# Kernel optimization log

Hardware: AMD Instinct MI355X
Metric: run time of the kernel (lower is better)

## Reference

```python
import jax, jax.numpy as jnp
import numpy as np
from jax import lax

DIM = 256
HEAD_DIM = 32
NUM_HEADS = DIM // HEAD_DIM
AGENT = 2
WIN = 7
DN = ('NCHW', 'OIHW', 'NCHW')


def _rpe_index(m, w):
    # faithful to torch buffer construction (meshgrid 'ij')
    coords = np.stack(np.meshgrid(np.arange(m), np.arange(w), np.arange(w), indexing='ij')).reshape(3, -1)
    rel = (coords[:, :, None] - coords[:, None, :]).transpose(1, 2, 0).astype(np.int64)
    rel[..., 0] += m - 1
    rel[..., 1] += w - 1
    rel[..., 2] += w - 1
    rel[..., 0] *= (2 * w - 1) * (2 * w - 1)
    rel[..., 1] *= 2 * w - 1
    return jnp.asarray(rel.sum(-1), dtype=jnp.int32)  # [N, N]


def _feat_extract(x, dw, se1, se2, pw):
    # depthwise 3x3 conv (groups=C, no bias)
    y = lax.conv_general_dilated(x, dw, (1, 1), [(1, 1), (1, 1)], dimension_numbers=DN,
                                 feature_group_count=x.shape[1])
    y = jax.nn.gelu(y, approximate=False)
    # SE block
    s = y.mean(axis=(2, 3))                                   # [B, C]
    s = jax.nn.sigmoid(jax.nn.gelu(s @ se1, approximate=False) @ se2)
    y = y * s[:, :, None, None]
    y = lax.conv_general_dilated(y, pw, (1, 1), [(0, 0), (0, 0)], dimension_numbers=DN)
    x = x + y
    # MaxPool2d(kernel=3, stride=2, padding=1)
    return lax.reduce_window(x, -jnp.inf, lax.max, (1, 1, 3, 3), (1, 1, 2, 2),
                             [(0, 0), (0, 0), (1, 1), (1, 1)])


def setup_inputs() -> dict:
    key = jax.random.key(0)
    ks = jax.random.split(key, 16)
    d, h, hd = DIM, NUM_HEADS, HEAD_DIM
    se_hidden = int(d * 0.25)
    rpe_rows = (2 * AGENT - 1) * (2 * WIN - 1) * (2 * WIN - 1)
    w = lambda k, shp: (jax.random.normal(k, shp, dtype=jnp.float32) * 0.02)
    return {
        'x': jax.random.normal(ks[0], (8, AGENT, 8, 8, WIN, WIN, d), dtype=jnp.float32),
        'qkv_w': w(ks[1], (d, 2 * d)),
        'qkv_b': jnp.zeros((2 * d,), dtype=jnp.float32),
        'to_out_w': w(ks[2], (d, d)),
        'rpe_table': w(ks[3], (rpe_rows, h)),
        'fe1_dw': w(ks[4], (d, 1, 3, 3)),
        'fe1_se1': w(ks[5], (d, se_hidden)),
        'fe1_se2': w(ks[6], (se_hidden, d)),
        'fe1_pw': w(ks[7], (d, d, 1, 1)),
        'fe2_dw': w(ks[8], (d, 1, 3, 3)),
        'fe2_se1': w(ks[9], (d, se_hidden)),
        'fe2_se2': w(ks[10], (se_hidden, d)),
        'fe2_pw': w(ks[11], (d, d, 1, 1)),
    }


def reference(x, qkv_w, qkv_b, to_out_w, rpe_table,
              fe1_dw, fe1_se1, fe1_se2, fe1_pw,
              fe2_dw, fe2_se1, fe2_se2, fe2_pw):
    b, m, gx, gy, w, _, d = x.shape
    h, hd = NUM_HEADS, HEAD_DIM
    scale = hd ** -0.5
    N = m * w * w

    # ---- global query path ----
    # 'b m x y w1 w2 d -> (b m) d (x w1) (y w2)'
    xg = x.transpose(0, 1, 6, 2, 4, 3, 5).reshape(b * m, d, gx * w, gy * w)
    xg = _feat_extract(xg, fe1_dw, fe1_se1, fe1_se2, fe1_pw)
    xg = _feat_extract(xg, fe2_dw, fe2_se1, fe2_se2, fe2_pw)
    C, H, W = xg.shape[1], xg.shape[2], xg.shape[3]
    nx, ny = H // w, W // w
    # '(b m) d (x w1) (y w2) -> b m x y w1 w2 d' then 'b l x y w1 w2 d -> b (x y) (l w1 w2) d'
    xg = xg.reshape(b, m, d, nx, w, ny, w).transpose(0, 3, 5, 1, 4, 6, 2).reshape(b, nx * ny, N, d)
    g_attn = jax.nn.softmax(jnp.einsum('bhid,bhjd->bhij', xg, xg)) * (C ** -0.5)
    xg = jnp.einsum('bhij,bhjd->bhid', g_attn, xg)
    q_global = xg.mean(axis=1)                                 # [b, N, d]
    q_global = q_global.reshape(b, N, h, hd).transpose(0, 2, 1, 3)  # [b, h, N, hd]

    # ---- window attention ----
    # 'b l x y w1 w2 d -> (b x y) (l w1 w2) d'
    xw = x.transpose(0, 2, 3, 1, 4, 5, 6).reshape(b * gx * gy, N, d)
    B_ = xw.shape[0]
    kv = (xw @ qkv_w + qkv_b).reshape(B_, N, 2, h, hd).transpose(2, 0, 3, 1, 4)
    k, v = kv[0], kv[1]                                        # [B_, h, N, hd]
    q = jnp.broadcast_to(q_global[:, None], (b, gx * gy, h, N, hd)).reshape(B_, h, N, hd)

    attn = jnp.einsum('bhid,bhjd->bhij', q * scale, k)         # [B_, h, N, N]
    idx = _rpe_index(m, w)                                     # [N, N] static int32
    bias = rpe_table[idx].transpose(2, 0, 1)                   # [h, N, N]
    attn = jax.nn.softmax(attn + bias[None])
    out = jnp.einsum('bhij,bhjd->bhid', attn, v)               # [B_, h, N, hd]

    # 'b h (l w1 w2) d -> b l w1 w2 (h d)'
    out = out.reshape(B_, h, m, w, w, hd).transpose(0, 2, 3, 4, 1, 5).reshape(B_, m, w, w, d)
    out = out @ to_out_w
    # '(b x y) l w1 w2 d -> b l x y w1 w2 d'
    return out.reshape(b, gx, gy, m, w, w, d).transpose(0, 3, 1, 2, 4, 5, 6)
```

## Files before the change

kernel.cpp:

```cpp
#include <hip/hip_runtime.h>


#define DEV static __device__ __forceinline__
typedef unsigned short u16;
typedef unsigned int u32;
typedef __attribute__((ext_vector_type(8))) short short8;
typedef __attribute__((ext_vector_type(4))) float f32x4;

DEV float b2f(u16 s) { union { u32 i; float f; } u; u.i = ((u32)s) << 16; return u.f; }
DEV u16 f2b(float f) {
    union { float f; u32 i; } u; u.f = f;
    u32 x = u.i;
    return (u16)((x + 0x7fffu + ((x >> 16) & 1u)) >> 16);
}
DEV u16 f2b_hw(float f) {
    __bf16 b = (__bf16)f;
    return __builtin_bit_cast(u16, b);
}
DEV float gelu_f(float x) { return 0.5f * x * (1.0f + erff(x * 0.70710678118654752440f)); }

DEV size_t x_rowbase(int r) {
    int b_ = r / 98, n = r % 98;
    int bb = b_ >> 6, gxi = (b_ >> 3) & 7, gyi = b_ & 7;
    int m = n / 49, rr = n % 49, w1 = rr / 7, w2 = rr % 7;
    return (((((size_t)(bb * 2 + m) * 8 + gxi) * 8 + gyi) * 7 + w1) * 7 + w2) * 256;
}

__global__ __launch_bounds__(256) void k_prep_both(const float* __restrict__ x, u16* __restrict__ xbf,
                                                   float* __restrict__ xg0) {
    int t = threadIdx.x;
    int s = blockIdx.x * 4 + (t >> 6);
    int c4 = (t & 63) << 2;
    int w2 = s % 7, t1 = s / 7;
    int w1 = t1 % 7, t2 = t1 / 7;
    int gy = t2 % 8, t3 = t2 / 8;
    int gx = t3 % 8, nm = t3 / 8;
    int m = nm & 1, bb = nm >> 1;
    int r  = (bb * 64 + gx * 8 + gy) * 98 + m * 49 + w1 * 7 + w2;
    int rg = nm * 3136 + (gx * 7 + w1) * 56 + gy * 7 + w2;
    float4 v = *(const float4*)(x + (size_t)s * 256 + c4);
    ushort4 o; o.x = f2b(v.x); o.y = f2b(v.y); o.z = f2b(v.z); o.w = f2b(v.w);
    *(ushort4*)(xbf + (size_t)r * 256 + c4) = o;
    *(float4*)(xg0 + (size_t)rg * 256 + c4) = v;
}

__global__ __launch_bounds__(256) void k_prep_w(const float* __restrict__ wq, const float* __restrict__ wo,
                                                const float* __restrict__ pw1, const float* __restrict__ pw2,
                                                const float* __restrict__ dw1, const float* __restrict__ dw2,
                                                u16* __restrict__ wqt, u16* __restrict__ wot,
                                                u16* __restrict__ pwb1, u16* __restrict__ pwb2,
                                                float* __restrict__ dwt1, float* __restrict__ dwt2) {
    int bid = blockIdx.x, t = threadIdx.x;
    if (bid < 512) {
        wqt[bid * 256 + t] = f2b(wq[(size_t)t * 512 + bid]);
    } else if (bid < 768) {
        int n = bid - 512;
        wot[n * 256 + t] = f2b(wo[(size_t)t * 256 + n]);
    } else if (bid < 1024) {
        int n = bid - 768;
        pwb1[n * 256 + t] = f2b(pw1[(size_t)n * 256 + t]);
    } else if (bid < 1280) {
        int n = bid - 1024;
        pwb2[n * 256 + t] = f2b(pw2[(size_t)n * 256 + t]);
    } else if (bid < 1289) {
        int k = bid - 1280;
        dwt1[k * 256 + t] = dw1[t * 9 + k];
    } else {
        int k = bid - 1289;
        dwt2[k * 256 + t] = dw2[t * 9 + k];
    }
}

__global__ __launch_bounds__(256) void k_bias(const float* __restrict__ rpe, float* __restrict__ biasf) {
    int u = blockIdx.x * 256 + threadIdx.x;
    int h = u / 10976, rem = u % 10976;
    int i = rem / 112, j = rem % 112;
    float v;
    if (j >= 98) {
        v = -1.0e38f;
    } else {
        int mi = (i >= 49), ri = i - 49 * mi, ai = ri / 7, bi = ri % 7;
        int mj = (j >= 49), rj = j - 49 * mj, aj = rj / 7, bj = rj % 7;
        int idx = ((mi - mj + 1) * 13 + (ai - aj + 6)) * 13 + (bi - bj + 6);
        v = rpe[idx * 8 + h];
    }
    biasf[u] = v;
}

DEV void gemm_tile(const u16* __restrict__ A, const u16* __restrict__ Bt,
                   int r0, int n0, int t, f32x4 acc[4][4],
                   u16 (*A_l)[72], u16 (*B_l)[72]) {
    int w = t >> 6, l = t & 63;
    int quad = l >> 4, lm = l & 15;
    int wm = (w & 1) * 64, wn = (w >> 1) * 64;
    for (int k0 = 0; k0 < 256; k0 += 64) {
        __syncthreads();
        #pragma unroll
        for (int i = 0; i < 4; i++) {
            int u = t + (i << 8);
            int row = u >> 3, k8 = (u & 7) << 3;
            *(uint4*)&A_l[row][k8] = *(const uint4*)(A + (size_t)(r0 + row) * 256 + k0 + k8);
            *(uint4*)&B_l[row][k8] = *(const uint4*)(Bt + (size_t)(n0 + row) * 256 + k0 + k8);
        }
        __syncthreads();
        #pragma unroll
        for (int kk = 0; kk < 64; kk += 32) {
            short8 af[4], bf[4];
            #pragma unroll
            for (int i = 0; i < 4; i++) af[i] = *(const short8*)&A_l[wm + 16 * i + lm][kk + quad * 8];
            #pragma unroll
            for (int j = 0; j < 4; j++) bf[j] = *(const short8*)&B_l[wn + 16 * j + lm][kk + quad * 8];
            #pragma unroll
            for (int i = 0; i < 4; i++)
                #pragma unroll
                for (int j = 0; j < 4; j++)
                    acc[i][j] = __builtin_amdgcn_mfma_f32_16x16x32_bf16(af[i], bf[j], acc[i][j], 0, 0, 0);
        }
    }
}

__global__ __launch_bounds__(256, 2) void k_gemm_qkv(const u16* __restrict__ A, const u16* __restrict__ Bt,
                                                     const float* __restrict__ bias, u16* __restrict__ C) {
    __shared__ u16 A_l[128][72];
    __shared__ u16 B_l[128][72];
    int r0 = blockIdx.x * 128, n0 = blockIdx.y * 128;
    int t = threadIdx.x;
    f32x4 acc[4][4] = {};
    gemm_tile(A, Bt, r0, n0, t, acc, A_l, B_l);
    int w = t >> 6, l = t & 63;
    int quad = l >> 4, lm = l & 15;
    int wm = (w & 1) * 64, wn = (w >> 1) * 64;
    float bj[4];
    #pragma unroll
    for (int j = 0; j < 4; j++) bj[j] = bias[n0 + wn + 16 * j + lm];
    #pragma unroll
    for (int i = 0; i < 4; i++) {
        int rbase = r0 + wm + 16 * i + quad * 4;
        #pragma unroll
        for (int reg = 0; reg < 4; reg++) {
            int row = rbase + reg;
            #pragma unroll
            for (int j = 0; j < 4; j++) {
                int c0 = n0 + wn + 16 * j;
                int slab = c0 >> 5;
                int dd = c0 & 31;
                C[((size_t)slab * 50176 + row) * 32 + dd + lm] = f2b(acc[i][j][reg] + bj[j]);
            }
        }
    }
}

__global__ __launch_bounds__(256, 2) void k_gemm_toout(const u16* __restrict__ A, const u16* __restrict__ Bt,
                                                       float* __restrict__ outp) {
    __shared__ u16 A_l[128][72];
    __shared__ u16 B_l[128][72];
    int r0 = blockIdx.x * 128, n0 = blockIdx.y * 128;
    int t = threadIdx.x;
    f32x4 acc[4][4] = {};
    gemm_tile(A, Bt, r0, n0, t, acc, A_l, B_l);
    int w = t >> 6, l = t & 63;
    int quad = l >> 4, lm = l & 15;
    int wm = (w & 1) * 64, wn = (w >> 1) * 64;
    #pragma unroll
    for (int i = 0; i < 4; i++) {
        int rbase = r0 + wm + 16 * i + quad * 4;
        #pragma unroll
        for (int reg = 0; reg < 4; reg++) {
            size_t ob = x_rowbase(rbase + reg);
            #pragma unroll
            for (int j = 0; j < 4; j++)
                outp[ob + n0 + wn + 16 * j + lm] = acc[i][j][reg];
        }
    }
}

__global__ __launch_bounds__(256) void k_scale_w(const u16* __restrict__ pwb, const float* __restrict__ ubuf,
                                                 u16* __restrict__ pwsc) {
    int b = blockIdx.x;
    int n = b >> 8, co = b & 255;
    int ci = threadIdx.x;
    pwsc[((size_t)b) * 256 + ci] = f2b(b2f(pwb[co * 256 + ci]) * ubuf[n * 256 + ci]);
}

template<int HW>
__global__ __launch_bounds__(256, 2) void k_pwconv_mfma_t(const u16* __restrict__ yT, const u16* __restrict__ pwsc,
                                                          float* __restrict__ base) {
    __shared__ u16 A_l[128][72];
    __shared__ u16 B_l[128][72];
    const int PX = (HW + 127) >> 7;
    int cpx = gridDim.x >> 3;
    int bid = (blockIdx.x & 7) * cpx + (blockIdx.x >> 3);
    int c0 = (bid & 1) * 128;
    int rem = bid >> 1;
    int p0 = (rem % PX) * 128;
    int n  = rem / PX;
    int t = threadIdx.x;
    const u16* A = yT + (size_t)n * HW * 256;
    const u16* Bt = pwsc + (size_t)n * 65536;
    f32x4 acc[4][4] = {};
    gemm_tile(A, Bt, p0, c0, t, acc, A_l, B_l);
    int w = t >> 6, l = t & 63;
    int quad = l >> 4, lm = l & 15;
    int wm = (w & 1) * 64, wn = (w >> 1) * 64;
    #pragma unroll
    for (int i = 0; i < 4; i++) {
        int pb = p0 + wm + 16 * i + quad * 4;
        #pragma unroll
        for (int reg = 0; reg < 4; reg++) {
            int p = pb + reg;
            if (p < HW) {
                size_t rowb = ((size_t)n * HW + p) * 256;
                #pragma unroll
                for (int j = 0; j < 4; j++)
                    base[rowb + c0 + wn + 16 * j + lm] += acc[i][j][reg];
            }
        }
    }
}

__global__ __launch_bounds__(256, 4) void k_attn_mfma(const u16* __restrict__ kv, const u16* __restrict__ qg,
                                                      const float* __restrict__ biasf, u16* __restrict__ ao) {
    __shared__ u16 K_l[112][40];
    __shared__ u16 Vt_l[32][136];
    __shared__ u16 P_l[4][16][136];
    int b_ = blockIdx.x, h = blockIdx.y;
    int bb = b_ >> 6;
    int t = threadIdx.x;

    const u16* kq = kv + ((size_t)h * 50176 + (size_t)b_ * 98) * 32;
    const u16* kvv = kv + ((size_t)(8 + h) * 50176 + (size_t)b_ * 98) * 32;
    const u16* qgn = qg + ((size_t)(bb * 8 + h) * 98) * 32;

    for (int u = t; u < 392; u += 256) {
        int row = u >> 2, q8 = (u & 3) << 3;
        *(short8*)&K_l[row][q8] = *(const short8*)(kq + u * 8);
    }
    for (int u = t; u < 224; u += 256) {
        int row = 98 + (u >> 4), c2 = (u & 15) << 1;
        *(u32*)&K_l[row][c2] = 0;
    }
    for (int u = t; u < 392; u += 256) {
        int j = u >> 2, c = u & 3;
        short8 v = *(const short8*)(kvv + u * 8);
        #pragma unroll
        for (int e = 0; e < 8; e++) Vt_l[c * 8 + e][j] = (u16)v[e];
    }
    for (int u = t; u < 1216; u += 256) {
        int d = u / 38, c = 98 + u % 38;
        Vt_l[d][c] = 0;
    }
    for (int u = t; u < 1536; u += 256) {
        int wv = u / 384, rem = u % 384;
        P_l[wv][rem / 24][112 + rem % 24] = 0;
    }
    __syncthreads();

    int w = t >> 6, l = t & 63;
    int quad = l >> 4, lm = l & 15;
    const float scale = 0.17677669529663688f;

    #pragma unroll
    for (int half = 0; half < 2; half++) {
        int mt = w + 4 * half;
        if (mt >= 7) break;
        int m0 = mt * 16;
        int qrow = m0 + lm; qrow = (qrow < 98) ? qrow : 97;
        const float* bp = biasf + (size_t)(h * 98 + qrow) * 112 + quad * 4;
        f32x4 b4[7];
        #pragma unroll
        for (int t6 = 0; t6 < 7; t6++) b4[t6] = *(const f32x4*)(bp + t6 * 16);
        short8 aq = *(const short8*)(qgn + qrow * 32 + quad * 8);
        f32x4 acc[7] = {};
        #pragma unroll
        for (int t6 = 0; t6 < 7; t6++) {
            short8 bk = *(const short8*)&K_l[t6 * 16 + lm][quad * 8];
            acc[t6] = __builtin_amdgcn_mfma_f32_16x16x32_bf16(bk, aq, acc[t6], 0, 0, 0);
        }
        float mx = -3.0e38f;
        #pragma unroll
        for (int t6 = 0; t6 < 7; t6++) {
            #pragma unroll
            for (int reg = 0; reg < 4; reg++) {
                float s = acc[t6][reg] * scale + b4[t6][reg];
                acc[t6][reg] = s;
                mx = fmaxf(mx, s);
            }
        }
        mx = fmaxf(mx, __shfl_xor(mx, 16));
        mx = fmaxf(mx, __shfl_xor(mx, 32));
        float sum = 0.f;
        #pragma unroll
        for (int t6 = 0; t6 < 7; t6++) {
            #pragma unroll
            for (int reg = 0; reg < 4; reg++) {
                float e = __expf(acc[t6][reg] - mx);
                acc[t6][reg] = e; sum += e;
            }
        }
        sum += __shfl_xor(sum, 16);
        sum += __shfl_xor(sum, 32);
        float inv = 1.0f / sum;
        #pragma unroll
        for (int t6 = 0; t6 < 7; t6++) {
            ushort4 s4;
            s4.x = f2b_hw(acc[t6][0] * inv);
            s4.y = f2b_hw(acc[t6][1] * inv);
            s4.z = f2b_hw(acc[t6][2] * inv);
            s4.w = f2b_hw(acc[t6][3] * inv);
            *(ushort4*)&P_l[w][lm][t6 * 16 + quad * 4] = s4;
        }
        __builtin_amdgcn_s_waitcnt(0);
        short8 pa[4];
        #pragma unroll
        for (int kc = 0; kc < 4; kc++)
            pa[kc] = *(const short8*)&P_l[w][lm][kc * 32 + quad * 8];
        #pragma unroll
        for (int nt = 0; nt < 2; nt++) {
            f32x4 oacc = {};
            #pragma unroll
            for (int kc = 0; kc < 4; kc++) {
                short8 bv = *(const short8*)&Vt_l[nt * 16 + lm][kc * 32 + quad * 8];
                oacc = __builtin_amdgcn_mfma_f32_16x16x32_bf16(pa[kc], bv, oacc, 0, 0, 0);
            }
            #pragma unroll
            for (int reg = 0; reg < 4; reg++) {
                int orow = m0 + quad * 4 + reg;
                if (orow < 98)
                    ao[((size_t)(b_ * 98 + orow)) * 256 + h * 32 + nt * 16 + lm] = f2b_hw(oacc[reg]);
            }
        }
    }
}

template<int HW, int WW>
__global__ __launch_bounds__(256) void k_dwconv_t(const float* __restrict__ in, const float* __restrict__ dwT,
                                                  u16* __restrict__ out) {
    const int HP = HW / 2;
    const int WP = WW / 2;
    int cpx = gridDim.x >> 3;
    int bid = (blockIdx.x & 7) * cpx + (blockIdx.x >> 3);
    int idx = bid * 256 + threadIdx.x;
    int c4 = (idx & 63) << 2;
    int pp = (idx >> 6) % HP;
    int n  = (idx >> 6) / HP;
    int i  = pp / WP, jp = (pp % WP) * 2;
    const float* base = in + (size_t)n * HW * 256 + c4;
    f32x4 w0[3], w1[3], w2[3];
    #pragma unroll
    for (int dy = 0; dy < 3; dy++) {
        w0[dy] = *(const f32x4*)(dwT + (dy * 3 + 0) * 256 + c4);
        w1[dy] = *(const f32x4*)(dwT + (dy * 3 + 1) * 256 + c4);
        w2[dy] = *(const f32x4*)(dwT + (dy * 3 + 2) * 256 + c4);
    }
    f32x4 acc0 = {}, acc1 = {};
    #pragma unroll
    for (int dy = 0; dy < 3; dy++) {
        int y = i + dy - 1;
        if (y < 0 || y >= WW) continue;
        const float* rowb = base + (size_t)(y * WW) * 256;
        f32x4 v1 = *(const f32x4*)(rowb + (size_t)jp * 256);
        f32x4 v2 = *(const f32x4*)(rowb + (size_t)(jp + 1) * 256);
        f32x4 v0 = (jp > 0) ? *(const f32x4*)(rowb + (size_t)(jp - 1) * 256) : (f32x4){};
        f32x4 v3 = (jp + 2 < WW) ? *(const f32x4*)(rowb + (size_t)(jp + 2) * 256) : (f32x4){};
        acc0 += v0 * w0[dy] + v1 * w1[dy] + v2 * w2[dy];
        acc1 += v1 * w0[dy] + v2 * w1[dy] + v3 * w2[dy];
    }
    ushort4 o0, o1;
    o0.x = f2b(gelu_f(acc0[0])); o0.y = f2b(gelu_f(acc0[1]));
    o0.z = f2b(gelu_f(acc0[2])); o0.w = f2b(gelu_f(acc0[3]));
    o1.x = f2b(gelu_f(acc1[0])); o1.y = f2b(gelu_f(acc1[1]));
    o1.z = f2b(gelu_f(acc1[2])); o1.w = f2b(gelu_f(acc1[3]));
    size_t ob = ((size_t)n * HW + (size_t)i * WW + jp) * 256 + c4;
    *(ushort4*)(out + ob) = o0;
    *(ushort4*)(out + ob + 256) = o1;
}

template<int HW>
__global__ __launch_bounds__(256) void k_chanmean_t(const u16* __restrict__ y, float* __restrict__ sbuf) {
    int n = blockIdx.x, sl = blockIdx.y;
    int c = threadIdx.x;
    const int PP = HW / 16;
    const u16* base = y + ((size_t)n * HW + sl * PP) * 256 + c;
    float s = 0.f;
    for (int p = 0; p < PP; p++) s += b2f(base[(size_t)p * 256]);
    atomicAdd(&sbuf[n * 256 + c], s);
}

__global__ __launch_bounds__(256) void k_se1(const float* __restrict__ sbuf, const float* __restrict__ se1,
                                             float* __restrict__ tbuf, float invHW) {
    int o = blockIdx.x * 256 + threadIdx.x;
    int n = o >> 6, j = o & 63;
    const float* srow = sbuf + n * 256;
    float acc = 0.f;
    for (int c = 0; c < 256; c++) acc += srow[c] * se1[c * 64 + j];
    tbuf[o] = gelu_f(acc * invHW);
}
__global__ __launch_bounds__(256) void k_se2(const float* __restrict__ tbuf, const float* __restrict__ se2,
                                             float* __restrict__ ubuf) {
    int o = blockIdx.x * 256 + threadIdx.x;
    int n = o >> 8, co = o & 255;
    const float* trow = tbuf + n * 64;
    float acc = 0.f;
    for (int j = 0; j < 64; j++) acc += trow[j] * se2[j * 256 + co];
    ubuf[o] = 1.0f / (1.0f + __expf(-acc));
}

template<int HI>
__global__ __launch_bounds__(256) void k_maxpool_t(const float* __restrict__ in, float* __restrict__ out) {
    const int HO = HI / 2;
    int cpx = gridDim.x >> 3;
    int bid = (blockIdx.x & 7) * cpx + (blockIdx.x >> 3);
    int idx = bid * 256 + threadIdx.x;
    int c4 = (idx & 63) << 2;
    int pp = (idx >> 6) % (HO * HO);
    int n = (idx >> 6) / (HO * HO);
    int j = pp % HO, i = pp / HO;
    const float* base = in + (size_t)n * HI * HI * 256 + c4;
    float mx = -3.0e38f, my = -3.0e38f, mz = -3.0e38f, mw = -3.0e38f;
    #pragma unroll
    for (int dr = 0; dr < 3; dr++) {
        int r = 2 * i - 1 + dr;
        if (r < 0 || r >= HI) continue;
        #pragma unroll
        for (int dc = 0; dc < 3; dc++) {
            int cc = 2 * j - 1 + dc;
            if (cc < 0 || cc >= HI) continue;
            float4 v = *(const float4*)(base + (size_t)(r * HI + cc) * 256);
            mx = fmaxf(mx, v.x); my = fmaxf(my, v.y);
            mz = fmaxf(mz, v.z); mw = fmaxf(mw, v.w);
        }
    }
    float4 o; o.x = mx; o.y = my; o.z = mz; o.w = mw;
    *(float4*)(out + (size_t)idx * 4) = o;
}

__global__ __launch_bounds__(256) void k_rearr_xg_t(const float* __restrict__ p2, float* __restrict__ xg) {
    int t = threadIdx.x;
    int r = blockIdx.x * 4 + (t >> 6);
    int c4 = (t & 63) << 2;
    int gihi = r / 98, n = r % 98;
    int b = gihi >> 2, gi = gihi & 3;
    int m = n / 49, rr = n % 49, w1 = rr / 7, w2 = rr % 7;
    int X = (gi >> 1) * 7 + w1, Y = (gi & 1) * 7 + w2;
    size_t src = ((size_t)((b * 2 + m) * 196 + X * 14 + Y)) * 256;
    *(float4*)(xg + (size_t)r * 256 + c4) = *(const float4*)(p2 + src + c4);
}

__global__ __launch_bounds__(256, 2) void k_gattn(const float* __restrict__ xg, float* __restrict__ qpart) {
    int rt = blockIdx.x, gi = blockIdx.y, b = blockIdx.z;
    __shared__ float A_l[98][68];
    __shared__ float S_l[14][100];
    int t = threadIdx.x;
    const float* Ab = xg + (size_t)(b * 4 + gi) * 98 * 256;
    int ti = t >> 5, tj = t & 31;
    int i1c = (ti + 8 < 14) ? ti + 8 : 13;
    int jc[4];
    #pragma unroll
    for (int jj = 0; jj < 4; jj++) { int j = tj + 32 * jj; jc[jj] = (j < 98) ? j : 97; }
    float accS[2][4] = {};
    for (int ch = 0; ch < 4; ch++) {
        __syncthreads();
        for (int u = t; u < 1568; u += 256) {
            int row = u >> 4, c4 = (u & 15) << 2;
            *(float4*)&A_l[row][c4] = *(const float4*)(Ab + row * 256 + ch * 64 + c4);
        }
        __syncthreads();
        for (int c4 = 0; c4 < 64; c4 += 4) {
            float4 ak[4];
            #pragma unroll
            for (int jj = 0; jj < 4; jj++) ak[jj] = *(const float4*)&A_l[jc[jj]][c4];
            float4 aq0 = *(const float4*)&A_l[rt * 14 + ti][c4];
            float4 aq1 = *(const float4*)&A_l[rt * 14 + i1c][c4];
            #pragma unroll
            for (int jj = 0; jj < 4; jj++) {
                accS[0][jj] += aq0.x * ak[jj].x + aq0.y * ak[jj].y + aq0.z * ak[jj].z + aq0.w * ak[jj].w;
                accS[1][jj] += aq1.x * ak[jj].x + aq1.y * ak[jj].y + aq1.z * ak[jj].z + aq1.w * ak[jj].w;
            }
        }
    }
    #pragma unroll
    for (int ii = 0; ii < 2; ii++) {
        int il = ti + 8 * ii;
        if (il < 14) {
            #pragma unroll
            for (int jj = 0; jj < 4; jj++) {
                int j = tj + 32 * jj;
                if (j < 98) S_l[il][j] = accS[ii][jj];
            }
        }
    }
    __syncthreads();
    {
        int g = t >> 4, l = t & 15;
        if (g < 14) {
            float mx = -3.0e38f;
            for (int jj = 0; jj < 7; jj++) { int j = l + 16 * jj; if (j < 98) mx = fmaxf(mx, S_l[g][j]); }
            #pragma unroll
            for (int off = 8; off > 0; off >>= 1) mx = fmaxf(mx, __shfl_xor(mx, off, 16));
            float sum = 0.f;
            for (int jj = 0; jj < 7; jj++) {
                int j = l + 16 * jj;
                if (j < 98) { float e = __expf(S_l[g][j] - mx); S_l[g][j] = e; sum += e; }
            }
            #pragma unroll
            for (int off = 8; off > 0; off >>= 1) sum += __shfl_xor(sum, off, 16);
            float inv = 0.0625f / sum;
            for (int jj = 0; jj < 7; jj++) { int j = l + 16 * jj; if (j < 98) S_l[g][j] *= inv; }
        }
    }
    __syncthreads();
    int ti2 = t >> 4, tc2 = t & 15;
    int rowv = (ti2 < 14);
    int ti2c = rowv ? ti2 : 13;
    size_t qrow = ((size_t)(b * 4 + gi) * 98 + rt * 14 + ti2c) * 256;
    for (int ch = 0; ch < 4; ch++) {
        __syncthreads();
        for (int u = t; u < 1568; u += 256) {
            int row = u >> 4, c4 = (u & 15) << 2;
            *(float4*)&A_l[row][c4] = *(const float4*)(Ab + row * 256 + ch * 64 + c4);
        }
        __syncthreads();
        float4 acc = make_float4(0.f, 0.f, 0.f, 0.f);
        for (int j0 = 0; j0 < 96; j0 += 4) {
            float s4[4];
            *(float4*)s4 = *(const float4*)&S_l[ti2c][j0];
            #pragma unroll
            for (int jj = 0; jj < 4; jj++) {
                float4 a = *(const float4*)&A_l[j0 + jj][tc2 * 4];
                acc.x += s4[jj] * a.x; acc.y += s4[jj] * a.y; acc.z += s4[jj] * a.z; acc.w += s4[jj] * a.w;
            }
        }
        #pragma unroll
        for (int j = 96; j < 98; j++) {
            float sv = S_l[ti2c][j];
            float4 a = *(const float4*)&A_l[j][tc2 * 4];
            acc.x += sv * a.x; acc.y += sv * a.y; acc.z += sv * a.z; acc.w += sv * a.w;
        }
        if (rowv) *(float4*)(qpart + qrow + ch * 64 + tc2 * 4) = acc;
    }
}

__global__ __launch_bounds__(256) void k_qmean(const float* __restrict__ qpart, u16* __restrict__ qg) {
    int u = blockIdx.x * 256 + threadIdx.x;
    int b = u / 6272, r = u % 6272;
    const float* bp = qpart + (size_t)b * 100352 + (size_t)r * 4;
    float4 a0 = *(const float4*)(bp);
    float4 a1 = *(const float4*)(bp + 25088);
    float4 a2 = *(const float4*)(bp + 50176);
    float4 a3 = *(const float4*)(bp + 75264);
    ushort4 o;
    o.x = f2b(0.25f * (a0.x + a1.x + a2.x + a3.x));
    o.y = f2b(0.25f * (a0.y + a1.y + a2.y + a3.y));
    o.z = f2b(0.25f * (a0.z + a1.z + a2.z + a3.z));
    o.w = f2b(0.25f * (a0.w + a1.w + a2.w + a3.w));
    int row = r >> 6;
    int c = (r & 63) * 4;
    int h = c >> 5, d0 = c & 31;
    *(ushort4*)(qg + ((size_t)(b * 8 + h) * 98 + row) * 32 + d0) = o;
}

extern "C" void kernel_launch(void* const* d_in, const int* in_sizes, int n_in,
                              void* d_out, int out_size, void* d_ws, size_t ws_size,
                              hipStream_t stream) {
    const float* x      = (const float*)d_in[0];
    const float* qkv_w  = (const float*)d_in[1];
    const float* qkv_b  = (const float*)d_in[2];
    const float* to_out = (const float*)d_in[3];
    const float* rpe    = (const float*)d_in[4];
    const float* fe1_dw = (const float*)d_in[5];
    const float* fe1_s1 = (const float*)d_in[6];
    const float* fe1_s2 = (const float*)d_in[7];
    const float* fe1_pw = (const float*)d_in[8];
    const float* fe2_dw = (const float*)d_in[9];
    const float* fe2_s1 = (const float*)d_in[10];
    const float* fe2_s2 = (const float*)d_in[11];
    const float* fe2_pw = (const float*)d_in[12];

    float* ws   = (float*)d_ws;
    float* xg0  = ws;
    u16*   ybuf = (u16*)(ws + 12845056);
    u16*   kvbf = (u16*)ws;
    u16*   aobf = (u16*)(ws + 12845056);
    u16*   xbf  = (u16*)(ws + 25690112);
    float* p1   = ws + 32112640;
    float* p2   = ws + 35323904;
    float* xgb  = ws + 36126720;
    float* qprt = ws + 36929536;
    u16*   qgbf = (u16*)(ws + 37732352);
    float* dwt1 = ws + 37832704;
    float* dwt2 = ws + 37835008;
    u16*   wqt  = (u16*)(ws + 37933056);
    u16*   wot  = (u16*)(ws + 37998592);
    float* sbuf = ws + 38031360;
    float* tbuf = ws + 38035456;
    float* ubuf = ws + 38036480;
    u16*   pwb1 = (u16*)(ws + 38040576);
    u16*   pwb2 = (u16*)(ws + 38073344);
    u16*   pwsc = (u16*)(ws + 38106112);
    float* biasf = qprt;

    k_prep_w<<<1298, 256, 0, stream>>>(qkv_w, to_out, fe1_pw, fe2_pw, fe1_dw, fe2_dw,
                                       wqt, wot, pwb1, pwb2, dwt1, dwt2);
    k_prep_both<<<12544, 256, 0, stream>>>(x, xbf, xg0);
    k_dwconv_t<3136, 56><<<6272, 256, 0, stream>>>(xg0, dwt1, ybuf);
    hipMemsetAsync(sbuf, 0, 16 * 256 * sizeof(float), stream);
    k_chanmean_t<3136><<<dim3(16, 16), 256, 0, stream>>>(ybuf, sbuf);
    k_se1<<<4, 256, 0, stream>>>(sbuf, fe1_s1, tbuf, 1.0f / 3136.0f);
    k_se2<<<16, 256, 0, stream>>>(tbuf, fe1_s2, ubuf);
    k_scale_w<<<4096, 256, 0, stream>>>(pwb1, ubuf, pwsc);
    k_pwconv_mfma_t<3136><<<800, 256, 0, stream>>>(ybuf, pwsc, xg0);
    k_maxpool_t<56><<<3136, 256, 0, stream>>>(xg0, p1);
    k_dwconv_t<784, 28><<<1568, 256, 0, stream>>>(p1, dwt2, ybuf);
    hipMemsetAsync(sbuf, 0, 16 * 256 * sizeof(float), stream);
    k_chanmean_t<784><<<dim3(16, 16), 256, 0, stream>>>(ybuf, sbuf);
    k_se1<<<4, 256, 0, stream>>>(sbuf, fe2_s1, tbuf, 1.0f / 784.0f);
    k_se2<<<16, 256, 0, stream>>>(tbuf, fe2_s2, ubuf);
    k_scale_w<<<4096, 256, 0, stream>>>(pwb2, ubuf, pwsc);
    k_pwconv_mfma_t<784><<<224, 256, 0, stream>>>(ybuf, pwsc, p1);
    k_maxpool_t<28><<<784, 256, 0, stream>>>(p1, p2);
    k_rearr_xg_t<<<784, 256, 0, stream>>>(p2, xgb);
    k_gattn<<<dim3(7, 4, 8), 256, 0, stream>>>(xgb, qprt);
    k_qmean<<<196, 256, 0, stream>>>(qprt, qgbf);
    k_bias<<<343, 256, 0, stream>>>(rpe, biasf);
    k_gemm_qkv<<<dim3(392, 4), 256, 0, stream>>>(xbf, wqt, qkv_b, kvbf);
    k_attn_mfma<<<dim3(512, 8), 256, 0, stream>>>(kvbf, qgbf, biasf, aobf);
    k_gemm_toout<<<dim3(392, 2), 256, 0, stream>>>(aobf, wot, (float*)d_out);
}
```

Measured before the change: 368.2 us.

## Fuse bf16 conversion of x into QKV GEMM and vectorize channel-mean reduction

The QKV GEMM now reads the fp32 input directly with the window-gather row mapping and converts to bf16 while staging into shared memory. This removes the separate bf16 copy of x that the prep kernel used to write and the GEMM used to read back. The trade-off is that each of the four column blocks re-reads fp32 x, which doubles the per-tile A-load bytes. Separately, the channel-mean kernel now uses 4-wide vector loads with an in-block shared-memory reduction before the atomics, in place of strided scalar loads.

```diff
diff --git a/kernel.cpp b/kernel.cpp
--- a/kernel.cpp
+++ b/kernel.cpp
@@ -26,8 +26,7 @@
     return (((((size_t)(bb * 2 + m) * 8 + gxi) * 8 + gyi) * 7 + w1) * 7 + w2) * 256;
 }
 
-__global__ __launch_bounds__(256) void k_prep_both(const float* __restrict__ x, u16* __restrict__ xbf,
-                                                   float* __restrict__ xg0) {
+__global__ __launch_bounds__(256) void k_prep_xg(const float* __restrict__ x, float* __restrict__ xg0) {
     int t = threadIdx.x;
     int s = blockIdx.x * 4 + (t >> 6);
     int c4 = (t & 63) << 2;
@@ -35,12 +34,8 @@
     int w1 = t1 % 7, t2 = t1 / 7;
     int gy = t2 % 8, t3 = t2 / 8;
     int gx = t3 % 8, nm = t3 / 8;
-    int m = nm & 1, bb = nm >> 1;
-    int r  = (bb * 64 + gx * 8 + gy) * 98 + m * 49 + w1 * 7 + w2;
     int rg = nm * 3136 + (gx * 7 + w1) * 56 + gy * 7 + w2;
     float4 v = *(const float4*)(x + (size_t)s * 256 + c4);
-    ushort4 o; o.x = f2b(v.x); o.y = f2b(v.y); o.z = f2b(v.z); o.w = f2b(v.w);
-    *(ushort4*)(xbf + (size_t)r * 256 + c4) = o;
     *(float4*)(xg0 + (size_t)rg * 256 + c4) = v;
 }
 
@@ -119,17 +114,54 @@
     }
 }
 
-__global__ __launch_bounds__(256, 2) void k_gemm_qkv(const u16* __restrict__ A, const u16* __restrict__ Bt,
+__global__ __launch_bounds__(256, 2) void k_gemm_qkv(const float* __restrict__ X, const u16* __restrict__ Bt,
                                                      const float* __restrict__ bias, u16* __restrict__ C) {
     __shared__ u16 A_l[128][72];
     __shared__ u16 B_l[128][72];
     int r0 = blockIdx.x * 128, n0 = blockIdx.y * 128;
     int t = threadIdx.x;
-    f32x4 acc[4][4] = {};
-    gemm_tile(A, Bt, r0, n0, t, acc, A_l, B_l);
     int w = t >> 6, l = t & 63;
     int quad = l >> 4, lm = l & 15;
     int wm = (w & 1) * 64, wn = (w >> 1) * 64;
+    size_t abase[4];
+    #pragma unroll
+    for (int i = 0; i < 4; i++) {
+        int u = t + (i << 8);
+        abase[i] = x_rowbase(r0 + (u >> 3)) + ((u & 7) << 3);
+    }
+    f32x4 acc[4][4] = {};
+    for (int k0 = 0; k0 < 256; k0 += 64) {
+        __syncthreads();
+        #pragma unroll
+        for (int i = 0; i < 4; i++) {
+            int u = t + (i << 8);
+            int row = u >> 3, k8 = (u & 7) << 3;
+            const float* s = X + abase[i] + k0;
+            float4 va = *(const float4*)s;
+            float4 vb = *(const float4*)(s + 4);
+            short8 pk;
+            pk[0] = (short)f2b_hw(va.x); pk[1] = (short)f2b_hw(va.y);
+            pk[2] = (short)f2b_hw(va.z); pk[3] = (short)f2b_hw(va.w);
+            pk[4] = (short)f2b_hw(vb.x); pk[5] = (short)f2b_hw(vb.y);
+            pk[6] = (short)f2b_hw(vb.z); pk[7] = (short)f2b_hw(vb.w);
+            *(short8*)&A_l[row][k8] = pk;
+            *(uint4*)&B_l[row][k8] = *(const uint4*)(Bt + (size_t)(n0 + row) * 256 + k0 + k8);
+        }
+        __syncthreads();
+        #pragma unroll
+        for (int kk = 0; kk < 64; kk += 32) {
+            short8 af[4], bf[4];
+            #pragma unroll
+            for (int i = 0; i < 4; i++) af[i] = *(const short8*)&A_l[wm + 16 * i + lm][kk + quad * 8];
+            #pragma unroll
+            for (int j = 0; j < 4; j++) bf[j] = *(const short8*)&B_l[wn + 16 * j + lm][kk + quad * 8];
+            #pragma unroll
+            for (int i = 0; i < 4; i++)
+                #pragma unroll
+                for (int j = 0; j < 4; j++)
+                    acc[i][j] = __builtin_amdgcn_mfma_f32_16x16x32_bf16(af[i], bf[j], acc[i][j], 0, 0, 0);
+        }
+    }
     float bj[4];
     #pragma unroll
     for (int j = 0; j < 4; j++) bj[j] = bias[n0 + wn + 16 * j + lm];
@@ -377,13 +409,29 @@
 
 template<int HW>
 __global__ __launch_bounds__(256) void k_chanmean_t(const u16* __restrict__ y, float* __restrict__ sbuf) {
+    __shared__ float4 red[256];
     int n = blockIdx.x, sl = blockIdx.y;
-    int c = threadIdx.x;
+    int t = threadIdx.x;
     const int PP = HW / 16;
-    const u16* base = y + ((size_t)n * HW + sl * PP) * 256 + c;
-    float s = 0.f;
-    for (int p = 0; p < PP; p++) s += b2f(base[(size_t)p * 256]);
-    atomicAdd(&sbuf[n * 256 + c], s);
+    int c4 = (t & 63) << 2;
+    int rr = t >> 6;
+    const u16* base = y + ((size_t)n * HW + sl * PP) * 256 + c4;
+    float sx = 0.f, sy = 0.f, sz = 0.f, sw = 0.f;
+    for (int p = rr; p < PP; p += 4) {
+        ushort4 v = *(const ushort4*)(base + (size_t)p * 256);
+        sx += b2f(v.x); sy += b2f(v.y); sz += b2f(v.z); sw += b2f(v.w);
+    }
+    float4 r; r.x = sx; r.y = sy; r.z = sz; r.w = sw;
+    red[t] = r;
+    __syncthreads();
+    if (t < 64) {
+        float4 a = red[t], b = red[t + 64], c = red[t + 128], d = red[t + 192];
+        float* sp = sbuf + n * 256 + (t << 2);
+        atomicAdd(sp + 0, a.x + b.x + c.x + d.x);
+        atomicAdd(sp + 1, a.y + b.y + c.y + d.y);
+        atomicAdd(sp + 2, a.z + b.z + c.z + d.z);
+        atomicAdd(sp + 3, a.w + b.w + c.w + d.w);
+    }
 }
 
 __global__ __launch_bounds__(256) void k_se1(const float* __restrict__ sbuf, const float* __restrict__ se1,
@@ -581,7 +629,6 @@
     u16*   ybuf = (u16*)(ws + 12845056);
     u16*   kvbf = (u16*)ws;
     u16*   aobf = (u16*)(ws + 12845056);
-    u16*   xbf  = (u16*)(ws + 25690112);
     float* p1   = ws + 32112640;
     float* p2   = ws + 35323904;
     float* xgb  = ws + 36126720;
@@ -601,7 +648,7 @@
 
     k_prep_w<<<1298, 256, 0, stream>>>(qkv_w, to_out, fe1_pw, fe2_pw, fe1_dw, fe2_dw,
                                        wqt, wot, pwb1, pwb2, dwt1, dwt2);
-    k_prep_both<<<12544, 256, 0, stream>>>(x, xbf, xg0);
+    k_prep_xg<<<12544, 256, 0, stream>>>(x, xg0);
     k_dwconv_t<3136, 56><<<6272, 256, 0, stream>>>(xg0, dwt1, ybuf);
     hipMemsetAsync(sbuf, 0, 16 * 256 * sizeof(float), stream);
     k_chanmean_t<3136><<<dim3(16, 16), 256, 0, stream>>>(ybuf, sbuf);
@@ -622,7 +669,7 @@
     k_gattn<<<dim3(7, 4, 8), 256, 0, stream>>>(xgb, qprt);
     k_qmean<<<196, 256, 0, stream>>>(qprt, qgbf);
     k_bias<<<343, 256, 0, stream>>>(rpe, biasf);
-    k_gemm_qkv<<<dim3(392, 4), 256, 0, stream>>>(xbf, wqt, qkv_b, kvbf);
+    k_gemm_qkv<<<dim3(392, 4), 256, 0, stream>>>(x, wqt, qkv_b, kvbf);
     k_attn_mfma<<<dim3(512, 8), 256, 0, stream>>>(kvbf, qgbf, biasf, aobf);
     k_gemm_toout<<<dim3(392, 2), 256, 0, stream>>>(aobf, wot, (float*)d_out);
 }
```

Result: slower. 383.4 us (+4.1%).
